# Kernel optimization log

Measured on AMD Instinct MI355X. Metric: run time of the kernel, lower is better.

Reference implementation:

```python
import jax, jax.numpy as jnp
import numpy as np
from jax import lax

EPS = 1e-6
TANH_CLIP = 1.0 - 1e-5
FRECHET_ITERS = 10


def _sqnorm(x):
    return jnp.sum(x * x, axis=-1, keepdims=True)


def _norm(x):
    return jnp.sqrt(jnp.clip(_sqnorm(x), EPS))


def _lambda(x, c):
    # conformal factor lambda_x = 2 / (1 - c ||x||^2)
    return 2.0 / jnp.clip(1.0 - c * _sqnorm(x), EPS)


def mobius_add(x, y, c):
    x2 = _sqnorm(x)
    y2 = _sqnorm(y)
    xy = jnp.sum(x * y, axis=-1, keepdims=True)
    num = (1.0 + 2.0 * c * xy + c * y2) * x + (1.0 - c * x2) * y
    den = 1.0 + 2.0 * c * xy + (c * c) * x2 * y2
    return num / jnp.clip(den, EPS)


def expmap(x, u, c):
    sc = jnp.sqrt(c)
    un = _norm(u)
    second = jnp.tanh(sc * _lambda(x, c) * un / 2.0) * u / (sc * un)
    return mobius_add(x, second, c)


def logmap(x, y, c):
    sc = jnp.sqrt(c)
    m = mobius_add(-x, y, c)
    mn = _norm(m)
    t = jnp.arctanh(jnp.clip(sc * mn, 0.0, TANH_CLIP))
    return (2.0 / (sc * _lambda(x, c))) * t * m / mn


def exp0(u, c):
    sc = jnp.sqrt(c)
    un = _norm(u)
    return jnp.tanh(sc * un) * u / (sc * un)


def dist(x, y, c):
    sc = jnp.sqrt(c)
    mn = _norm(mobius_add(-x, y, c))
    return (2.0 / sc) * jnp.arctanh(jnp.clip(sc * mn, 0.0, TANH_CLIP))[..., 0]


def gyr(a, b, w, c):
    # gyr[a,b]w = -(a (+) b) (+) (a (+) (b (+) w))
    return mobius_add(-mobius_add(a, b, c), mobius_add(a, mobius_add(b, w, c), c), c)


def transp(x, y, u, c):
    # parallel transport x -> y:  (lam_x / lam_y) * gyr[y, -x] u
    return (_lambda(x, c) / _lambda(y, c)) * gyr(y, -x, u, c)


def frechet_mean(x, c):
    # Karcher fixed-point iteration: mu <- exp_mu(mean_i log_mu(x_i))
    m = jnp.mean(x, axis=0)  # (D,)
    max_norm = (1.0 - 1e-3) / jnp.sqrt(c)
    mn = _norm(m)[0]
    m = m * jnp.minimum(1.0, max_norm / mn)

    def step(mu, _):
        g = jnp.mean(logmap(mu, x, c), axis=0)
        return expmap(mu, g, c), None

    mu, _ = lax.scan(step, m, None, length=FRECHET_ITERS)
    return mu


def setup_inputs() -> dict:
    key = jax.random.key(0)
    k1, k2 = jax.random.split(key)
    B, S, D = 64, 256, 256
    K = jnp.float32(-1.2)
    sc = np.sqrt(1.2)
    x = jax.random.normal(k1, (B, S, D), dtype=jnp.float32)
    # project points strictly inside the Poincare ball of radius 1/sqrt(c)
    x = x / (1.0 + _norm(x)) * jnp.float32(0.7 / sc)
    mean_param = 0.01 * jax.random.normal(k2, (D,), dtype=jnp.float32)
    var_param = jnp.float32(1.0)
    return {"x": x, "K": K, "mean_param": mean_param, "var_param": var_param}


def reference(x, K, mean_param, var_param):
    c = -K  # positive ball curvature (K = -1.2)
    shapes = x.shape
    xf = x.reshape(-1, shapes[-1])  # (N, D)
    on_manifold = exp0(mean_param, c)          # (D,) target mean on manifold
    mu = frechet_mean(xf, c)                   # (D,) batch Frechet mean
    var = jnp.mean(dist(xf, mu, c) ** 2)       # Frechet variance (scalar)
    logm = transp(mu, on_manifold, logmap(mu, xf, c), c)  # (N, D)
    logm = jnp.sqrt(var_param / (var + 1e-6)) * logm
    out = expmap(on_manifold, logm, c)         # (N, D)
    return out.reshape(shapes)
```

## Files before the change

kernel.cpp:

```cpp
#include <hip/hip_runtime.h>
#include <math.h>
#include <string.h>

#define EPSF 1e-6f
#define TCLIP (1.0f - 1e-5f)
#define NPTS 16384
#define DDIM 256
#define NBLK 128
#define NTHR 1024
#define PPB 128
#define NWAVE 16
#define PPW 8
#define PSTR 260
#define FRECHET_ITERS_N 10

#define WS_PA 64
#define WS_PB (WS_PA + NBLK * PSTR)

__device__ __forceinline__ void st_pair_sc1(float* addr, float a, float b) {
    float2 f2 = make_float2(a, b);
    double dv; memcpy(&dv, &f2, 8);
    __hip_atomic_store((double*)addr, dv, __ATOMIC_RELAXED, __HIP_MEMORY_SCOPE_AGENT);
}
__device__ __forceinline__ float2 ld_pair_sc1(const float* addr) {
    double dv = __hip_atomic_load((const double*)addr, __ATOMIC_RELAXED, __HIP_MEMORY_SCOPE_AGENT);
    float2 f2; memcpy(&f2, &dv, 8);
    return f2;
}
__device__ __forceinline__ void st_f_sc1(float* addr, float v) {
    __hip_atomic_store(addr, v, __ATOMIC_RELAXED, __HIP_MEMORY_SCOPE_AGENT);
}
__device__ __forceinline__ float ld_f_sc1(const float* addr) {
    return __hip_atomic_load(addr, __ATOMIC_RELAXED, __HIP_MEMORY_SCOPE_AGENT);
}
__device__ __forceinline__ void st_u_sc1(unsigned* addr, unsigned v) {
    __hip_atomic_store(addr, v, __ATOMIC_RELAXED, __HIP_MEMORY_SCOPE_AGENT);
}
__device__ __forceinline__ unsigned ld_u_sc1(const unsigned* addr) {
    return __hip_atomic_load(addr, __ATOMIC_RELAXED, __HIP_MEMORY_SCOPE_AGENT);
}

__device__ __forceinline__ float block_sum(float v) {
    __shared__ float s_bs[NWAVE];
    #pragma unroll
    for (int off = 32; off; off >>= 1) v += __shfl_xor(v, off);
    const int w = threadIdx.x >> 6, l = threadIdx.x & 63;
    __syncthreads();
    if (l == 0) s_bs[w] = v;
    __syncthreads();
    float s = 0.f;
    #pragma unroll
    for (int i = 0; i < NWAVE; ++i) s += s_bs[i];
    return s;
}

__global__ void init_tags(float* ws) {
    int t = threadIdx.x;
    if (t < NBLK) {
        st_u_sc1((unsigned*)(ws + WS_PA + t * PSTR + 258), 0u);
        st_u_sc1((unsigned*)(ws + WS_PB + t * PSTR + 258), 0u);
    }
}

__global__ __launch_bounds__(NTHR, 1) void rbn_fused(
    const float* __restrict__ x, const float* __restrict__ Kp,
    const float* __restrict__ mean_param, const float* __restrict__ var_param,
    float* __restrict__ out, float* __restrict__ ws)
{
    const float c = -Kp[0];
    const float sc = sqrtf(c);
    const float N1 = 1.f / NPTS;
    const int t = threadIdx.x, lane = t & 63, wv = t >> 6;
    const int b = blockIdx.x;
    const int p0 = b * PPB;
    const float4* xr = ((const float4*)x) + p0 * 64;

    float* PA = ws + WS_PA;
    float* PB = ws + WS_PB;

    __shared__ float mu_s[DDIM], om_s[DDIM];
    __shared__ float dpart[PPB * 65];
    __shared__ float dqr[PPB * 9];
    __shared__ float y2_s[PPB], e_s[PPB], d_s[PPB], w_s[PPB], sA_s[PPB], fx_s[PPB];
    __shared__ float pseg[NWAVE * DDIM];
    __shared__ float part1[NWAVE], part2[NWAVE], part3[NWAVE];

    unsigned barno = 0;

    float4 xreg[PPW];
    #pragma unroll
    for (int i = 0; i < PPW; ++i)
        xreg[i] = xr[(wv * PPW + i) * 64 + lane];

    auto poll_tags = [&](const float* buf) {
        if (t < NBLK) {
            const unsigned* tg = (const unsigned*)(buf + t * PSTR + 258);
            while (ld_u_sc1(tg) < barno)
                __builtin_amdgcn_s_sleep(1);
        }
        __syncthreads();
    };

    {
        float u = (t < DDIM) ? mean_param[t] : 0.f;
        float un2 = block_sum(u * u);
        float un = sqrtf(fmaxf(un2, EPSF));
        if (t < DDIM) om_s[t] = tanhf(sc * un) * u / (sc * un);
    }
    float om2;
    { float v = (t < DDIM) ? om_s[t] * om_s[t] : 0.f; om2 = block_sum(v); }

    ++barno;
    {
        float4 a = make_float4(0.f, 0.f, 0.f, 0.f);
        #pragma unroll
        for (int i = 0; i < PPW; ++i) {
            a.x += xreg[i].x; a.y += xreg[i].y; a.z += xreg[i].z; a.w += xreg[i].w;
        }
        __syncthreads();
        ((float4*)(pseg + wv * DDIM))[lane] = a;
        __syncthreads();
        float s = 0.f;
        if (t < DDIM) {
            #pragma unroll
            for (int w = 0; w < NWAVE; ++w) s += pseg[w * DDIM + t];
        }
        float partner = __shfl_xor(s, 1);
        if (t < DDIM && !(t & 1)) st_pair_sc1(PA + b * PSTR + t, s, partner);
        __syncthreads();
        if (t == 0) st_u_sc1((unsigned*)(PA + b * PSTR + 258), barno);
    }
    {
        #pragma unroll
        for (int i = 0; i < PPW; ++i) {
            float4 xv = xreg[i];
            dpart[(wv * PPW + i) * 65 + lane] =
                xv.x * xv.x + xv.y * xv.y + xv.z * xv.z + xv.w * xv.w;
        }
        __syncthreads();
        { int pl = t & 127, q = t >> 7; float s = 0.f;
          #pragma unroll
          for (int j = 0; j < 8; ++j) s += dpart[pl * 65 + q * 8 + j];
          dqr[pl * 9 + q] = s; }
        __syncthreads();
        if (t < PPB) { float s = 0.f;
            #pragma unroll
            for (int j = 0; j < 8; ++j) s += dqr[t * 9 + j];
            y2_s[t] = s; }
        __syncthreads();
        float4 om4 = ((const float4*)om_s)[lane];
        #pragma unroll
        for (int i = 0; i < PPW; ++i) {
            float4 xv = xreg[i];
            dpart[(wv * PPW + i) * 65 + lane] =
                xv.x * om4.x + xv.y * om4.y + xv.z * om4.z + xv.w * om4.w;
        }
        __syncthreads();
        { int pl = t & 127, q = t >> 7; float s = 0.f;
          #pragma unroll
          for (int j = 0; j < 8; ++j) s += dpart[pl * 65 + q * 8 + j];
          dqr[pl * 9 + q] = s; }
        __syncthreads();
        if (t < PPB) { float s = 0.f;
            #pragma unroll
            for (int j = 0; j < 8; ++j) s += dqr[t * 9 + j];
            e_s[t] = s; }
    }
    poll_tags(PA);

    float mu2;
    {
        const int dg = t & 127, sg = t >> 7;
        float ax = 0.f, ay = 0.f;
        #pragma unroll
        for (int j = 0; j < 16; ++j) {
            float2 v = ld_pair_sc1(PA + (sg * 16 + j) * PSTR + 2 * dg);
            ax += v.x; ay += v.y;
        }
        __syncthreads();
        ((float2*)(pseg + sg * DDIM))[dg] = make_float2(ax, ay);
        __syncthreads();
        float m = 0.f, mm = 0.f;
        if (t < DDIM) {
            float s = 0.f;
            #pragma unroll
            for (int w = 0; w < 8; ++w) s += pseg[w * DDIM + t];
            m = s * N1; mm = m * m;
        }
        #pragma unroll
        for (int off = 32; off; off >>= 1) mm += __shfl_xor(mm, off);
        if (lane == 0) part1[wv] = mm;
        __syncthreads();
        float mn2 = 0.f;
        #pragma unroll
        for (int i = 0; i < NWAVE; ++i) mn2 += part1[i];
        float mn = sqrtf(fmaxf(mn2, EPSF));
        float maxn = (1.f - 1e-3f) / sc;
        float f = fminf(1.f, maxn / mn);
        if (t < DDIM) mu_s[t] = m * f;
        mu2 = f * f * mn2;
        __syncthreads();
    }

    for (int it = 0; it < FRECHET_ITERS_N; ++it) {
        float* buf = (it & 1) ? PA : PB;
        ++barno;
        float4 mu4 = ((const float4*)mu_s)[lane];
        #pragma unroll
        for (int i = 0; i < PPW; ++i) {
            float4 xv = xreg[i];
            dpart[(wv * PPW + i) * 65 + lane] =
                xv.x * mu4.x + xv.y * mu4.y + xv.z * mu4.z + xv.w * mu4.w;
        }
        __syncthreads();
        { int pl = t & 127, q = t >> 7; float s = 0.f;
          #pragma unroll
          for (int j = 0; j < 8; ++j) s += dpart[pl * 65 + q * 8 + j];
          dqr[pl * 9 + q] = s; }
        __syncthreads();
        float sAv = 0.f, wdv = 0.f;
        if (t < PPB) {
            float d = 0.f;
            #pragma unroll
            for (int j = 0; j < 8; ++j) d += dqr[t * 9 + j];
            float y2 = y2_s[t];
            float P = 1.f - 2.f * c * d;
            float den = fmaxf(P + c * c * mu2 * y2, EPSF);
            float A = -(P + c * y2) / den;
            float B = (1.f - c * mu2) / den;
            float mn2 = fmaxf(A * A * mu2 + 2.f * A * B * d + B * B * y2, EPSF);
            float mn = sqrtf(mn2);
            float tt = atanhf(fminf(sc * mn, TCLIP));
            float s = (fmaxf(1.f - c * mu2, EPSF) / sc) * tt / mn;
            float w = s * B;
            w_s[t] = w;
            sAv = s * A;
            wdv = w * d;
        }
        __syncthreads();
        {
            float4 a = make_float4(0.f, 0.f, 0.f, 0.f);
            #pragma unroll
            for (int i = 0; i < PPW; ++i) {
                float w = w_s[wv * PPW + i];
                a.x += w * xreg[i].x; a.y += w * xreg[i].y;
                a.z += w * xreg[i].z; a.w += w * xreg[i].w;
            }
            ((float4*)(pseg + wv * DDIM))[lane] = a;
            #pragma unroll
            for (int off = 32; off; off >>= 1) {
                sAv += __shfl_xor(sAv, off); wdv += __shfl_xor(wdv, off);
            }
            if (lane == 0) { part1[wv] = sAv; part2[wv] = wdv; }
        }
        __syncthreads();
        {
            float s = 0.f;
            if (t < DDIM) {
                #pragma unroll
                for (int w = 0; w < NWAVE; ++w) s += pseg[w * DDIM + t];
            }
            float partner = __shfl_xor(s, 1);
            if (t < DDIM && !(t & 1)) st_pair_sc1(buf + b * PSTR + t, s, partner);
            if (t == 0) {
                float sa = 0.f, wd = 0.f;
                #pragma unroll
                for (int i = 0; i < NWAVE; ++i) { sa += part1[i]; wd += part2[i]; }
                st_pair_sc1(buf + b * PSTR + 256, sa, wd);
            }
        }
        __syncthreads();
        if (t == 0) st_u_sc1((unsigned*)(buf + b * PSTR + 258), barno);
        poll_tags(buf);
        const int dg = t & 127, sg = t >> 7;
        float ax = 0.f, ay = 0.f;
        #pragma unroll
        for (int j = 0; j < 16; ++j) {
            float2 v = ld_pair_sc1(buf + (sg * 16 + j) * PSTR + 2 * dg);
            ax += v.x; ay += v.y;
        }
        float2 sp = make_float2(0.f, 0.f);
        if (t < NBLK) sp = ld_pair_sc1(buf + t * PSTR + 256);
        ((float2*)(pseg + sg * DDIM))[dg] = make_float2(ax, ay);
        __syncthreads();
        float g = 0.f, vvv = 0.f;
        if (t < DDIM) {
            #pragma unroll
            for (int w = 0; w < 8; ++w) g += pseg[w * DDIM + t];
            vvv = g * g;
        }
        float sAt = sp.x, wdt = sp.y;
        #pragma unroll
        for (int off = 32; off; off >>= 1) {
            vvv += __shfl_xor(vvv, off); sAt += __shfl_xor(sAt, off); wdt += __shfl_xor(wdt, off);
        }
        if (lane == 0) { part1[wv] = vvv; part2[wv] = sAt; part3[wv] = wdt; }
        __syncthreads();
        float vv = 0.f, sa = 0.f, wd = 0.f;
        #pragma unroll
        for (int i = 0; i < NWAVE; ++i) { vv += part1[i]; sa += part2[i]; wd += part3[i]; }
        float gn2 = N1 * N1 * (vv + 2.f * sa * wd + sa * sa * mu2);
        float mg  = N1 * (wd + sa * mu2);
        float un = sqrtf(fmaxf(gn2, EPSF));
        float lam = 2.f / fmaxf(1.f - c * mu2, EPSF);
        float k = tanhf(sc * lam * un * 0.5f) / (sc * un);
        float ms = k * mg;
        float s2 = k * k * gn2;
        float aa = 1.f + 2.f * c * ms + c * s2;
        float bb2 = 1.f - c * mu2;
        float den = fmaxf(1.f + 2.f * c * ms + c * c * mu2 * s2, EPSF);
        float cm = (aa + bb2 * k * N1 * sa) / den;
        float cv = (bb2 * k * N1) / den;
        if (t < DDIM) mu_s[t] = cm * mu_s[t] + cv * g;
        mu2 = cm * cm * mu2 + 2.f * cm * cv * wd + cv * cv * vv;
        __syncthreads();
    }

    float* vbuf = ((FRECHET_ITERS_N - 1) & 1) ? PB : PA;
    ++barno;
    {
        float4 mu4 = ((const float4*)mu_s)[lane];
        #pragma unroll
        for (int i = 0; i < PPW; ++i) {
            float4 xv = xreg[i];
            dpart[(wv * PPW + i) * 65 + lane] =
                xv.x * mu4.x + xv.y * mu4.y + xv.z * mu4.z + xv.w * mu4.w;
        }
        __syncthreads();
        { int pl = t & 127, q = t >> 7; float s = 0.f;
          #pragma unroll
          for (int j = 0; j < 8; ++j) s += dpart[pl * 65 + q * 8 + j];
          dqr[pl * 9 + q] = s; }
        __syncthreads();
        float vval = 0.f;
        if (t < PPB) {
            float d = 0.f;
            #pragma unroll
            for (int j = 0; j < 8; ++j) d += dqr[t * 9 + j];
            d_s[t] = d;
            float y2 = y2_s[t];
            float P = 1.f - 2.f * c * d;
            float den = fmaxf(P + c * c * mu2 * y2, EPSF);
            float A = -(P + c * y2) / den;
            float B = (1.f - c * mu2) / den;
            float mn2 = fmaxf(A * A * mu2 + 2.f * A * B * d + B * B * y2, EPSF);
            float mn = sqrtf(mn2);
            float tt = atanhf(fminf(sc * mn, TCLIP));
            float dd = (2.f / sc) * tt;
            vval = dd * dd;
        }
        float ov = (t < DDIM) ? om_s[t] * mu_s[t] : 0.f;
        #pragma unroll
        for (int off = 32; off; off >>= 1) {
            vval += __shfl_xor(vval, off); ov += __shfl_xor(ov, off);
        }
        if (lane == 0) { part1[wv] = vval; part2[wv] = ov; }
        __syncthreads();
        if (t == 0) {
            float tot = 0.f;
            #pragma unroll
            for (int i = 0; i < NWAVE; ++i) tot += part1[i];
            st_f_sc1(vbuf + b * PSTR + 256, tot);
        }
        __syncthreads();
        if (t == 0) st_u_sc1((unsigned*)(vbuf + b * PSTR + 258), barno);
    }
    float omu = 0.f;
    #pragma unroll
    for (int i = 0; i < NWAVE; ++i) omu += part2[i];

    const float Amu = fmaxf(1.f - c * mu2, EPSF);
    const float Aom = fmaxf(1.f - c * om2, EPSF);
    const float ratio = Aom / Amu;
    const float aq = 1.f - 2.f * c * omu + c * mu2;
    const float bq = 1.f - c * om2;
    const float dqv = fmaxf(1.f - 2.f * c * omu + c * c * om2 * mu2, EPSF);
    const float qo = aq / dqv, qm = -bq / dqv;
    const float q2 = qo * qo * om2 + 2.f * qo * qm * omu + qm * qm * mu2;
    const float lam_om = 2.f / Aom;

    if (t < PPB) {
        float y2 = y2_s[t], d = d_s[t], e = e_s[t];
        auto dotOm3 = [&](float po, float pm, float px) { return po * om2 + pm * omu + px * e; };
        auto dotMu3 = [&](float po, float pm, float px) { return po * omu + pm * mu2 + px * d; };
        auto sqn3 = [&](float po, float pm, float px) {
            return po * po * om2 + pm * pm * mu2 + px * px * y2
                 + 2.f * (po * pm * omu + po * px * e + pm * px * d);
        };
        float P = 1.f - 2.f * c * d;
        float den0 = fmaxf(P + c * c * mu2 * y2, EPSF);
        float A = -(P + c * y2) / den0;
        float B = (1.f - c * mu2) / den0;
        float mn2 = fmaxf(A * A * mu2 + 2.f * A * B * d + B * B * y2, EPSF);
        float mn = sqrtf(mn2);
        float tt = atanhf(fminf(sc * mn, TCLIP));
        float s = (fmaxf(1.f - c * mu2, EPSF) / sc) * tt / mn;
        float Um = s * A, Ux = s * B;

        float xy1 = -dotMu3(0.f, Um, Ux);
        float Y21 = sqn3(0.f, Um, Ux);
        float a1 = 1.f + 2.f * c * xy1 + c * Y21;
        float b1 = 1.f - c * mu2;
        float dn1 = fmaxf(1.f + 2.f * c * xy1 + c * c * mu2 * Y21, EPSF);
        float h1m = (-a1 + b1 * Um) / dn1;
        float h1x = (b1 * Ux) / dn1;

        float xy2 = dotOm3(0.f, h1m, h1x);
        float Y22 = sqn3(0.f, h1m, h1x);
        float a2 = 1.f + 2.f * c * xy2 + c * Y22;
        float b2 = 1.f - c * om2;
        float dn2 = fmaxf(1.f + 2.f * c * xy2 + c * c * om2 * Y22, EPSF);
        float h2o = a2 / dn2;
        float h2m = (b2 * h1m) / dn2;
        float h2x = (b2 * h1x) / dn2;

        float xy3 = -(qo * dotOm3(h2o, h2m, h2x) + qm * dotMu3(h2o, h2m, h2x));
        float Y23 = sqn3(h2o, h2m, h2x);
        float a3 = 1.f + 2.f * c * xy3 + c * Y23;
        float b3 = 1.f - c * q2;
        float dn3 = fmaxf(1.f + 2.f * c * xy3 + c * c * q2 * Y23, EPSF);
        w_s[t]  = (-a3 * qo + b3 * h2o) / dn3;
        sA_s[t] = (-a3 * qm + b3 * h2m) / dn3;
        fx_s[t] = (b3 * h2x) / dn3;
    }
    poll_tags(vbuf);

    float va = (t < NBLK) ? ld_f_sc1(vbuf + t * PSTR + 256) : 0.f;
    #pragma unroll
    for (int off = 32; off; off >>= 1) va += __shfl_xor(va, off);
    if (lane == 0) part1[wv] = va;
    __syncthreads();
    float vsum = 0.f;
    #pragma unroll
    for (int i = 0; i < NWAVE; ++i) vsum += part1[i];
    float var = vsum * N1;
    float gamma = sqrtf(var_param[0] / (var + 1e-6f));

    if (t < PPB) {
        float y2 = y2_s[t], d = d_s[t], e = e_s[t];
        float g2o = w_s[t], g2m = sA_s[t], g2x = fx_s[t];
        float k1 = ratio * gamma;
        float Lo = k1 * g2o, Lm = k1 * g2m, Lx = k1 * g2x;
        float un2 = Lo * Lo * om2 + Lm * Lm * mu2 + Lx * Lx * y2
                  + 2.f * (Lo * Lm * omu + Lo * Lx * e + Lm * Lx * d);
        float un = sqrtf(fmaxf(un2, EPSF));
        float coef = tanhf(sc * lam_om * un * 0.5f) / (sc * un);
        float So = coef * Lo, Sm = coef * Lm, Sx = coef * Lx;
        float xy4 = So * om2 + Sm * omu + Sx * e;
        float Y24 = coef * coef * un2;
        float a4 = 1.f + 2.f * c * xy4 + c * Y24;
        float b4 = 1.f - c * om2;
        float dn4 = fmaxf(1.f + 2.f * c * xy4 + c * c * om2 * Y24, EPSF);
        w_s[t]  = (a4 + b4 * So) / dn4;
        sA_s[t] = (b4 * Sm) / dn4;
        fx_s[t] = (b4 * Sx) / dn4;
    }
    __syncthreads();

    {
        float4 mu4f = ((const float4*)mu_s)[lane];
        float4 om4f = ((const float4*)om_s)[lane];
        #pragma unroll
        for (int i = 0; i < PPW; ++i) {
            int pl = wv * PPW + i;
            float fo = w_s[pl], fm = sA_s[pl], fx = fx_s[pl];
            float4 x4 = xreg[i];
            float4 o4;
            o4.x = fo * om4f.x + fm * mu4f.x + fx * x4.x;
            o4.y = fo * om4f.y + fm * mu4f.y + fx * x4.y;
            o4.z = fo * om4f.z + fm * mu4f.z + fx * x4.z;
            o4.w = fo * om4f.w + fm * mu4f.w + fx * x4.w;
            ((float4*)out)[(p0 + pl) * 64 + lane] = o4;
        }
    }
}

extern "C" void kernel_launch(void* const* d_in, const int* in_sizes, int n_in,
                              void* d_out, int out_size, void* d_ws, size_t ws_size,
                              hipStream_t stream) {
    const float* x = (const float*)d_in[0];
    const float* K = (const float*)d_in[1];
    const float* mean_param = (const float*)d_in[2];
    const float* var_param = (const float*)d_in[3];
    float* out = (float*)d_out;
    float* ws = (float*)d_ws;

    init_tags<<<1, 256, 0, stream>>>(ws);
    void* args[] = {(void*)&x, (void*)&K, (void*)&mean_param, (void*)&var_param,
                    (void*)&out, (void*)&ws};
    hipLaunchCooperativeKernel((const void*)rbn_fused, dim3(NBLK), dim3(NTHR),
                               args, 0, stream);
}
```

Before: 188.1 us.

## Make per-point dot products wave-local, replacing block-wide reductions and barriers

Each wave now reduces the dot products for its own 8 points using a per-wave LDS slice plus shuffle-xor, and keeps the per-point scalars (y2, e, d, weights) in registers instead of block-shared arrays. This removes several __syncthreads per Frechet iteration and in the prologue and epilogue, along with the shared staging arrays. Per-point coefficients reach the weighted sums through lane shuffles. Every lane in a group of 8 redundantly computes the scalar math, so the transcendental work per point is duplicated across lanes, and wave-level sums have to divide by the redundancy correctly.

```diff
diff --git a/kernel.cpp b/kernel.cpp
--- a/kernel.cpp
+++ b/kernel.cpp
@@ -12,6 +12,7 @@
 #define NWAVE 16
 #define PPW 8
 #define PSTR 260
+#define WSLICE (PPW * 65)
 #define FRECHET_ITERS_N 10
 
 #define WS_PA 64
@@ -79,9 +80,7 @@
     float* PB = ws + WS_PB;
 
     __shared__ float mu_s[DDIM], om_s[DDIM];
-    __shared__ float dpart[PPB * 65];
-    __shared__ float dqr[PPB * 9];
-    __shared__ float y2_s[PPB], e_s[PPB], d_s[PPB], w_s[PPB], sA_s[PPB], fx_s[PPB];
+    __shared__ float dpart[NWAVE * WSLICE];
     __shared__ float pseg[NWAVE * DDIM];
     __shared__ float part1[NWAVE], part2[NWAVE], part3[NWAVE];
 
@@ -91,6 +90,28 @@
     #pragma unroll
     for (int i = 0; i < PPW; ++i)
         xreg[i] = xr[(wv * PPW + i) * 64 + lane];
+
+    auto wave_dot = [&](float4 v4, bool self) -> float {
+        float* slice = dpart + wv * WSLICE;
+        #pragma unroll
+        for (int i = 0; i < PPW; ++i) {
+            float4 xv = xreg[i];
+            float4 u4 = self ? xv : v4;
+            slice[i * 65 + lane] = xv.x * u4.x + xv.y * u4.y + xv.z * u4.z + xv.w * u4.w;
+        }
+        const int g = lane >> 3, q = lane & 7;
+        float s = 0.f;
+        #pragma unroll
+        for (int j = 0; j < 8; ++j) s += slice[g * 65 + q * 8 + j];
+        #pragma unroll
+        for (int off = 1; off <= 4; off <<= 1) s += __shfl_xor(s, off);
+        return s;
+    };
+    auto wave_sum_groups = [&](float v) -> float {
+        #pragma unroll
+        for (int off = 8; off <= 32; off <<= 1) v += __shfl_xor(v, off);
+        return v;
+    };
 
     auto poll_tags = [&](const float* buf) {
         if (t < NBLK) {
@@ -117,9 +138,10 @@
         for (int i = 0; i < PPW; ++i) {
             a.x += xreg[i].x; a.y += xreg[i].y; a.z += xreg[i].z; a.w += xreg[i].w;
         }
-        __syncthreads();
         ((float4*)(pseg + wv * DDIM))[lane] = a;
-        __syncthreads();
+    }
+    __syncthreads();
+    {
         float s = 0.f;
         if (t < DDIM) {
             #pragma unroll
@@ -127,44 +149,15 @@
         }
         float partner = __shfl_xor(s, 1);
         if (t < DDIM && !(t & 1)) st_pair_sc1(PA + b * PSTR + t, s, partner);
-        __syncthreads();
-        if (t == 0) st_u_sc1((unsigned*)(PA + b * PSTR + 258), barno);
-    }
-    {
-        #pragma unroll
-        for (int i = 0; i < PPW; ++i) {
-            float4 xv = xreg[i];
-            dpart[(wv * PPW + i) * 65 + lane] =
-                xv.x * xv.x + xv.y * xv.y + xv.z * xv.z + xv.w * xv.w;
-        }
-        __syncthreads();
-        { int pl = t & 127, q = t >> 7; float s = 0.f;
-          #pragma unroll
-          for (int j = 0; j < 8; ++j) s += dpart[pl * 65 + q * 8 + j];
-          dqr[pl * 9 + q] = s; }
-        __syncthreads();
-        if (t < PPB) { float s = 0.f;
-            #pragma unroll
-            for (int j = 0; j < 8; ++j) s += dqr[t * 9 + j];
-            y2_s[t] = s; }
-        __syncthreads();
+    }
+    __syncthreads();
+    if (t == 0) st_u_sc1((unsigned*)(PA + b * PSTR + 258), barno);
+
+    float y2r = wave_dot(make_float4(0.f, 0.f, 0.f, 0.f), true);
+    float er;
+    {
         float4 om4 = ((const float4*)om_s)[lane];
-        #pragma unroll
-        for (int i = 0; i < PPW; ++i) {
-            float4 xv = xreg[i];
-            dpart[(wv * PPW + i) * 65 + lane] =
-                xv.x * om4.x + xv.y * om4.y + xv.z * om4.z + xv.w * om4.w;
-        }
-        __syncthreads();
-        { int pl = t & 127, q = t >> 7; float s = 0.f;
-          #pragma unroll
-          for (int j = 0; j < 8; ++j) s += dpart[pl * 65 + q * 8 + j];
-          dqr[pl * 9 + q] = s; }
-        __syncthreads();
-        if (t < PPB) { float s = 0.f;
-            #pragma unroll
-            for (int j = 0; j < 8; ++j) s += dqr[t * 9 + j];
-            e_s[t] = s; }
+        er = wave_dot(om4, false);
     }
     poll_tags(PA);
 
@@ -177,7 +170,6 @@
             float2 v = ld_pair_sc1(PA + (sg * 16 + j) * PSTR + 2 * dg);
             ax += v.x; ay += v.y;
         }
-        __syncthreads();
         ((float2*)(pseg + sg * DDIM))[dg] = make_float2(ax, ay);
         __syncthreads();
         float m = 0.f, mm = 0.f;
@@ -206,24 +198,10 @@
         float* buf = (it & 1) ? PA : PB;
         ++barno;
         float4 mu4 = ((const float4*)mu_s)[lane];
-        #pragma unroll
-        for (int i = 0; i < PPW; ++i) {
-            float4 xv = xreg[i];
-            dpart[(wv * PPW + i) * 65 + lane] =
-                xv.x * mu4.x + xv.y * mu4.y + xv.z * mu4.z + xv.w * mu4.w;
-        }
-        __syncthreads();
-        { int pl = t & 127, q = t >> 7; float s = 0.f;
-          #pragma unroll
-          for (int j = 0; j < 8; ++j) s += dpart[pl * 65 + q * 8 + j];
-          dqr[pl * 9 + q] = s; }
-        __syncthreads();
-        float sAv = 0.f, wdv = 0.f;
-        if (t < PPB) {
-            float d = 0.f;
-            #pragma unroll
-            for (int j = 0; j < 8; ++j) d += dqr[t * 9 + j];
-            float y2 = y2_s[t];
+        float d = wave_dot(mu4, false);
+        float w, sA;
+        {
+            float y2 = y2r;
             float P = 1.f - 2.f * c * d;
             float den = fmaxf(P + c * c * mu2 * y2, EPSF);
             float A = -(P + c * y2) / den;
@@ -232,33 +210,28 @@
             float mn = sqrtf(mn2);
             float tt = atanhf(fminf(sc * mn, TCLIP));
             float s = (fmaxf(1.f - c * mu2, EPSF) / sc) * tt / mn;
-            float w = s * B;
-            w_s[t] = w;
-            sAv = s * A;
-            wdv = w * d;
-        }
-        __syncthreads();
+            w = s * B;
+            sA = s * A;
+        }
         {
             float4 a = make_float4(0.f, 0.f, 0.f, 0.f);
             #pragma unroll
             for (int i = 0; i < PPW; ++i) {
-                float w = w_s[wv * PPW + i];
-                a.x += w * xreg[i].x; a.y += w * xreg[i].y;
-                a.z += w * xreg[i].z; a.w += w * xreg[i].w;
+                float wi = __shfl(w, i * 8);
+                a.x += wi * xreg[i].x; a.y += wi * xreg[i].y;
+                a.z += wi * xreg[i].z; a.w += wi * xreg[i].w;
             }
             ((float4*)(pseg + wv * DDIM))[lane] = a;
-            #pragma unroll
-            for (int off = 32; off; off >>= 1) {
-                sAv += __shfl_xor(sAv, off); wdv += __shfl_xor(wdv, off);
-            }
-            if (lane == 0) { part1[wv] = sAv; part2[wv] = wdv; }
-        }
+        }
+        float sAw = wave_sum_groups(sA);
+        float wdw = wave_sum_groups(w * d);
+        if (lane == 0) { part1[wv] = sAw; part2[wv] = wdw; }
         __syncthreads();
         {
             float s = 0.f;
             if (t < DDIM) {
                 #pragma unroll
-                for (int w = 0; w < NWAVE; ++w) s += pseg[w * DDIM + t];
+                for (int w2 = 0; w2 < NWAVE; ++w2) s += pseg[w2 * DDIM + t];
             }
             float partner = __shfl_xor(s, 1);
             if (t < DDIM && !(t & 1)) st_pair_sc1(buf + b * PSTR + t, s, partner);
@@ -286,7 +259,7 @@
         float g = 0.f, vvv = 0.f;
         if (t < DDIM) {
             #pragma unroll
-            for (int w = 0; w < 8; ++w) g += pseg[w * DDIM + t];
+            for (int w2 = 0; w2 < 8; ++w2) g += pseg[w2 * DDIM + t];
             vvv = g * g;
         }
         float sAt = sp.x, wdt = sp.y;
@@ -318,53 +291,39 @@
 
     float* vbuf = ((FRECHET_ITERS_N - 1) & 1) ? PB : PA;
     ++barno;
-    {
-        float4 mu4 = ((const float4*)mu_s)[lane];
-        #pragma unroll
-        for (int i = 0; i < PPW; ++i) {
-            float4 xv = xreg[i];
-            dpart[(wv * PPW + i) * 65 + lane] =
-                xv.x * mu4.x + xv.y * mu4.y + xv.z * mu4.z + xv.w * mu4.w;
-        }
-        __syncthreads();
-        { int pl = t & 127, q = t >> 7; float s = 0.f;
-          #pragma unroll
-          for (int j = 0; j < 8; ++j) s += dpart[pl * 65 + q * 8 + j];
-          dqr[pl * 9 + q] = s; }
-        __syncthreads();
-        float vval = 0.f;
-        if (t < PPB) {
-            float d = 0.f;
-            #pragma unroll
-            for (int j = 0; j < 8; ++j) d += dqr[t * 9 + j];
-            d_s[t] = d;
-            float y2 = y2_s[t];
-            float P = 1.f - 2.f * c * d;
-            float den = fmaxf(P + c * c * mu2 * y2, EPSF);
-            float A = -(P + c * y2) / den;
-            float B = (1.f - c * mu2) / den;
-            float mn2 = fmaxf(A * A * mu2 + 2.f * A * B * d + B * B * y2, EPSF);
-            float mn = sqrtf(mn2);
-            float tt = atanhf(fminf(sc * mn, TCLIP));
-            float dd = (2.f / sc) * tt;
-            vval = dd * dd;
-        }
+    float4 mu4f = ((const float4*)mu_s)[lane];
+    float4 om4f = ((const float4*)om_s)[lane];
+    float d = wave_dot(mu4f, false);
+    float vval;
+    {
+        float y2 = y2r;
+        float P = 1.f - 2.f * c * d;
+        float den = fmaxf(P + c * c * mu2 * y2, EPSF);
+        float A = -(P + c * y2) / den;
+        float B = (1.f - c * mu2) / den;
+        float mn2 = fmaxf(A * A * mu2 + 2.f * A * B * d + B * B * y2, EPSF);
+        float mn = sqrtf(mn2);
+        float tt = atanhf(fminf(sc * mn, TCLIP));
+        float dd = (2.f / sc) * tt;
+        vval = dd * dd;
+    }
+    {
+        float vw = wave_sum_groups(vval);
         float ov = (t < DDIM) ? om_s[t] * mu_s[t] : 0.f;
         #pragma unroll
-        for (int off = 32; off; off >>= 1) {
-            vval += __shfl_xor(vval, off); ov += __shfl_xor(ov, off);
-        }
-        if (lane == 0) { part1[wv] = vval; part2[wv] = ov; }
-        __syncthreads();
-        if (t == 0) {
-            float tot = 0.f;
-            #pragma unroll
-            for (int i = 0; i < NWAVE; ++i) tot += part1[i];
-            st_f_sc1(vbuf + b * PSTR + 256, tot);
-        }
-        __syncthreads();
-        if (t == 0) st_u_sc1((unsigned*)(vbuf + b * PSTR + 258), barno);
-    }
+        for (int off = 32; off; off >>= 1) ov += __shfl_xor(ov, off);
+        if (lane == 0) { part1[wv] = vw; part2[wv] = ov; }
+    }
+    __syncthreads();
+    if (t == 0) {
+        float tot = 0.f;
+        #pragma unroll
+        for (int i = 0; i < NWAVE; ++i) tot += part1[i];
+        st_f_sc1(vbuf + b * PSTR + 256, tot);
+    }
+    __syncthreads();
+    if (t == 0) st_u_sc1((unsigned*)(vbuf + b * PSTR + 258), barno);
+
     float omu = 0.f;
     #pragma unroll
     for (int i = 0; i < NWAVE; ++i) omu += part2[i];
@@ -379,8 +338,9 @@
     const float q2 = qo * qo * om2 + 2.f * qo * qm * omu + qm * qm * mu2;
     const float lam_om = 2.f / Aom;
 
-    if (t < PPB) {
-        float y2 = y2_s[t], d = d_s[t], e = e_s[t];
+    float g2o, g2m, g2x;
+    {
+        float y2 = y2r, e = er;
         auto dotOm3 = [&](float po, float pm, float px) { return po * om2 + pm * omu + px * e; };
         auto dotMu3 = [&](float po, float pm, float px) { return po * omu + pm * mu2 + px * d; };
         auto sqn3 = [&](float po, float pm, float px) {
@@ -419,16 +379,18 @@
         float a3 = 1.f + 2.f * c * xy3 + c * Y23;
         float b3 = 1.f - c * q2;
         float dn3 = fmaxf(1.f + 2.f * c * xy3 + c * c * q2 * Y23, EPSF);
-        w_s[t]  = (-a3 * qo + b3 * h2o) / dn3;
-        sA_s[t] = (-a3 * qm + b3 * h2m) / dn3;
-        fx_s[t] = (b3 * h2x) / dn3;
+        g2o = (-a3 * qo + b3 * h2o) / dn3;
+        g2m = (-a3 * qm + b3 * h2m) / dn3;
+        g2x = (b3 * h2x) / dn3;
     }
     poll_tags(vbuf);
 
-    float va = (t < NBLK) ? ld_f_sc1(vbuf + t * PSTR + 256) : 0.f;
-    #pragma unroll
-    for (int off = 32; off; off >>= 1) va += __shfl_xor(va, off);
-    if (lane == 0) part1[wv] = va;
+    {
+        float va = (t < NBLK) ? ld_f_sc1(vbuf + t * PSTR + 256) : 0.f;
+        #pragma unroll
+        for (int off = 32; off; off >>= 1) va += __shfl_xor(va, off);
+        if (lane == 0) part1[wv] = va;
+    }
     __syncthreads();
     float vsum = 0.f;
     #pragma unroll
@@ -436,9 +398,9 @@
     float var = vsum * N1;
     float gamma = sqrtf(var_param[0] / (var + 1e-6f));
 
-    if (t < PPB) {
-        float y2 = y2_s[t], d = d_s[t], e = e_s[t];
-        float g2o = w_s[t], g2m = sA_s[t], g2x = fx_s[t];
+    float fo, fm, fx;
+    {
+        float y2 = y2r, e = er;
         float k1 = ratio * gamma;
         float Lo = k1 * g2o, Lm = k1 * g2m, Lx = k1 * g2x;
         float un2 = Lo * Lo * om2 + Lm * Lm * mu2 + Lx * Lx * y2
@@ -451,27 +413,23 @@
         float a4 = 1.f + 2.f * c * xy4 + c * Y24;
         float b4 = 1.f - c * om2;
         float dn4 = fmaxf(1.f + 2.f * c * xy4 + c * c * om2 * Y24, EPSF);
-        w_s[t]  = (a4 + b4 * So) / dn4;
-        sA_s[t] = (b4 * Sm) / dn4;
-        fx_s[t] = (b4 * Sx) / dn4;
-    }
-    __syncthreads();
-
-    {
-        float4 mu4f = ((const float4*)mu_s)[lane];
-        float4 om4f = ((const float4*)om_s)[lane];
-        #pragma unroll
-        for (int i = 0; i < PPW; ++i) {
-            int pl = wv * PPW + i;
-            float fo = w_s[pl], fm = sA_s[pl], fx = fx_s[pl];
-            float4 x4 = xreg[i];
-            float4 o4;
-            o4.x = fo * om4f.x + fm * mu4f.x + fx * x4.x;
-            o4.y = fo * om4f.y + fm * mu4f.y + fx * x4.y;
-            o4.z = fo * om4f.z + fm * mu4f.z + fx * x4.z;
-            o4.w = fo * om4f.w + fm * mu4f.w + fx * x4.w;
-            ((float4*)out)[(p0 + pl) * 64 + lane] = o4;
-        }
+        fo = (a4 + b4 * So) / dn4;
+        fm = (b4 * Sm) / dn4;
+        fx = (b4 * Sx) / dn4;
+    }
+
+    #pragma unroll
+    for (int i = 0; i < PPW; ++i) {
+        float foi = __shfl(fo, i * 8);
+        float fmi = __shfl(fm, i * 8);
+        float fxi = __shfl(fx, i * 8);
+        float4 x4 = xreg[i];
+        float4 o4;
+        o4.x = foi * om4f.x + fmi * mu4f.x + fxi * x4.x;
+        o4.y = foi * om4f.y + fmi * mu4f.y + fxi * x4.y;
+        o4.z = foi * om4f.z + fmi * mu4f.z + fxi * x4.z;
+        o4.w = foi * om4f.w + fmi * mu4f.w + fxi * x4.w;
+        ((float4*)out)[(p0 + wv * PPW + i) * 64 + lane] = o4;
     }
 }
 
```

New measurement: 194.0 us. 1.03x slower.

## Replace all-to-all grid reduction with single reducer block and broadcast tag

Applied to the files above, without the earlier changes.

Before, every block polled all 128 partial tags and re-read every block's partial sums to do the same reduction. Now block 0 alone gathers the partials, computes the updated mean (or the variance) and publishes it with one broadcast tag that the other blocks poll. Local per-block work (y2/e dot products, the transport coefficients) runs while waiting. The double-buffered partials and the separate tag-init kernel are dropped; equality polling on reused tags replaces them. The cost is an extra gather-then-broadcast hop on each iteration's critical path, plus some reliance on stale tag values never matching the expected phase.

```diff
diff --git a/kernel.cpp b/kernel.cpp
--- a/kernel.cpp
+++ b/kernel.cpp
@@ -13,9 +13,10 @@
 #define PPW 8
 #define PSTR 260
 #define FRECHET_ITERS_N 10
-
-#define WS_PA 64
-#define WS_PB (WS_PA + NBLK * PSTR)
+#define REDB 0
+
+#define WS_MU 64
+#define WS_PA (WS_MU + PSTR)
 
 __device__ __forceinline__ void st_pair_sc1(float* addr, float a, float b) {
     float2 f2 = make_float2(a, b);
@@ -52,14 +53,6 @@
     #pragma unroll
     for (int i = 0; i < NWAVE; ++i) s += s_bs[i];
     return s;
-}
-
-__global__ void init_tags(float* ws) {
-    int t = threadIdx.x;
-    if (t < NBLK) {
-        st_u_sc1((unsigned*)(ws + WS_PA + t * PSTR + 258), 0u);
-        st_u_sc1((unsigned*)(ws + WS_PB + t * PSTR + 258), 0u);
-    }
 }
 
 __global__ __launch_bounds__(NTHR, 1) void rbn_fused(
@@ -75,8 +68,9 @@
     const int p0 = b * PPB;
     const float4* xr = ((const float4*)x) + p0 * 64;
 
+    float* MU = ws + WS_MU;
     float* PA = ws + WS_PA;
-    float* PB = ws + WS_PB;
+    unsigned* MUtag = (unsigned*)(MU + 258);
 
     __shared__ float mu_s[DDIM], om_s[DDIM];
     __shared__ float dpart[PPB * 65];
@@ -84,21 +78,54 @@
     __shared__ float y2_s[PPB], e_s[PPB], d_s[PPB], w_s[PPB], sA_s[PPB], fx_s[PPB];
     __shared__ float pseg[NWAVE * DDIM];
     __shared__ float part1[NWAVE], part2[NWAVE], part3[NWAVE];
-
-    unsigned barno = 0;
+    __shared__ float bc[2];
+
+    unsigned p = 0;
 
     float4 xreg[PPW];
     #pragma unroll
     for (int i = 0; i < PPW; ++i)
         xreg[i] = xr[(wv * PPW + i) * 64 + lane];
 
-    auto poll_tags = [&](const float* buf) {
-        if (t < NBLK) {
-            const unsigned* tg = (const unsigned*)(buf + t * PSTR + 258);
-            while (ld_u_sc1(tg) < barno)
-                __builtin_amdgcn_s_sleep(1);
-        }
-        __syncthreads();
+    auto poll_eq = [&](const unsigned* tg, unsigned want) {
+        while (ld_u_sc1(tg) != want) __builtin_amdgcn_s_sleep(1);
+    };
+
+    auto compute_y2e = [&]() {
+        #pragma unroll
+        for (int i = 0; i < PPW; ++i) {
+            float4 xv = xreg[i];
+            dpart[(wv * PPW + i) * 65 + lane] =
+                xv.x * xv.x + xv.y * xv.y + xv.z * xv.z + xv.w * xv.w;
+        }
+        __syncthreads();
+        { int pl = t & 127, q = t >> 7; float s = 0.f;
+          #pragma unroll
+          for (int j = 0; j < 8; ++j) s += dpart[pl * 65 + q * 8 + j];
+          dqr[pl * 9 + q] = s; }
+        __syncthreads();
+        if (t < PPB) { float s = 0.f;
+            #pragma unroll
+            for (int j = 0; j < 8; ++j) s += dqr[t * 9 + j];
+            y2_s[t] = s; }
+        __syncthreads();
+        float4 om4 = ((const float4*)om_s)[lane];
+        #pragma unroll
+        for (int i = 0; i < PPW; ++i) {
+            float4 xv = xreg[i];
+            dpart[(wv * PPW + i) * 65 + lane] =
+                xv.x * om4.x + xv.y * om4.y + xv.z * om4.z + xv.w * om4.w;
+        }
+        __syncthreads();
+        { int pl = t & 127, q = t >> 7; float s = 0.f;
+          #pragma unroll
+          for (int j = 0; j < 8; ++j) s += dpart[pl * 65 + q * 8 + j];
+          dqr[pl * 9 + q] = s; }
+        __syncthreads();
+        if (t < PPB) { float s = 0.f;
+            #pragma unroll
+            for (int j = 0; j < 8; ++j) s += dqr[t * 9 + j];
+            e_s[t] = s; }
     };
 
     {
@@ -110,16 +137,17 @@
     float om2;
     { float v = (t < DDIM) ? om_s[t] * om_s[t] : 0.f; om2 = block_sum(v); }
 
-    ++barno;
+    ++p;
     {
         float4 a = make_float4(0.f, 0.f, 0.f, 0.f);
         #pragma unroll
         for (int i = 0; i < PPW; ++i) {
             a.x += xreg[i].x; a.y += xreg[i].y; a.z += xreg[i].z; a.w += xreg[i].w;
         }
-        __syncthreads();
         ((float4*)(pseg + wv * DDIM))[lane] = a;
-        __syncthreads();
+    }
+    __syncthreads();
+    {
         float s = 0.f;
         if (t < DDIM) {
             #pragma unroll
@@ -127,49 +155,14 @@
         }
         float partner = __shfl_xor(s, 1);
         if (t < DDIM && !(t & 1)) st_pair_sc1(PA + b * PSTR + t, s, partner);
-        __syncthreads();
-        if (t == 0) st_u_sc1((unsigned*)(PA + b * PSTR + 258), barno);
-    }
-    {
-        #pragma unroll
-        for (int i = 0; i < PPW; ++i) {
-            float4 xv = xreg[i];
-            dpart[(wv * PPW + i) * 65 + lane] =
-                xv.x * xv.x + xv.y * xv.y + xv.z * xv.z + xv.w * xv.w;
-        }
-        __syncthreads();
-        { int pl = t & 127, q = t >> 7; float s = 0.f;
-          #pragma unroll
-          for (int j = 0; j < 8; ++j) s += dpart[pl * 65 + q * 8 + j];
-          dqr[pl * 9 + q] = s; }
-        __syncthreads();
-        if (t < PPB) { float s = 0.f;
-            #pragma unroll
-            for (int j = 0; j < 8; ++j) s += dqr[t * 9 + j];
-            y2_s[t] = s; }
-        __syncthreads();
-        float4 om4 = ((const float4*)om_s)[lane];
-        #pragma unroll
-        for (int i = 0; i < PPW; ++i) {
-            float4 xv = xreg[i];
-            dpart[(wv * PPW + i) * 65 + lane] =
-                xv.x * om4.x + xv.y * om4.y + xv.z * om4.z + xv.w * om4.w;
-        }
-        __syncthreads();
-        { int pl = t & 127, q = t >> 7; float s = 0.f;
-          #pragma unroll
-          for (int j = 0; j < 8; ++j) s += dpart[pl * 65 + q * 8 + j];
-          dqr[pl * 9 + q] = s; }
-        __syncthreads();
-        if (t < PPB) { float s = 0.f;
-            #pragma unroll
-            for (int j = 0; j < 8; ++j) s += dqr[t * 9 + j];
-            e_s[t] = s; }
-    }
-    poll_tags(PA);
+    }
+    __syncthreads();
+    if (t == 0) st_u_sc1((unsigned*)(PA + b * PSTR + 258), p);
 
     float mu2;
-    {
+    if (b == REDB) {
+        if (t < NBLK) poll_eq((const unsigned*)(PA + t * PSTR + 258), p);
+        __syncthreads();
         const int dg = t & 127, sg = t >> 7;
         float ax = 0.f, ay = 0.f;
         #pragma unroll
@@ -177,7 +170,6 @@
             float2 v = ld_pair_sc1(PA + (sg * 16 + j) * PSTR + 2 * dg);
             ax += v.x; ay += v.y;
         }
-        __syncthreads();
         ((float2*)(pseg + sg * DDIM))[dg] = make_float2(ax, ay);
         __syncthreads();
         float m = 0.f, mm = 0.f;
@@ -197,14 +189,23 @@
         float mn = sqrtf(fmaxf(mn2, EPSF));
         float maxn = (1.f - 1e-3f) / sc;
         float f = fminf(1.f, maxn / mn);
-        if (t < DDIM) mu_s[t] = m * f;
+        if (t < DDIM) { float nm = m * f; mu_s[t] = nm; st_f_sc1(MU + t, nm); }
         mu2 = f * f * mn2;
+        if (t == 0) st_f_sc1(MU + 256, mu2);
+        __syncthreads();
+        if (t == 0) st_u_sc1(MUtag, p);
+        compute_y2e();
+    } else {
+        compute_y2e();
+        if (t == 0) { poll_eq(MUtag, p); bc[0] = ld_f_sc1(MU + 256); }
+        __syncthreads();
+        if (t < DDIM) mu_s[t] = ld_f_sc1(MU + t);
+        mu2 = bc[0];
         __syncthreads();
     }
 
     for (int it = 0; it < FRECHET_ITERS_N; ++it) {
-        float* buf = (it & 1) ? PA : PB;
-        ++barno;
+        ++p;
         float4 mu4 = ((const float4*)mu_s)[lane];
         #pragma unroll
         for (int i = 0; i < PPW; ++i) {
@@ -258,113 +259,128 @@
             float s = 0.f;
             if (t < DDIM) {
                 #pragma unroll
-                for (int w = 0; w < NWAVE; ++w) s += pseg[w * DDIM + t];
+                for (int w2 = 0; w2 < NWAVE; ++w2) s += pseg[w2 * DDIM + t];
             }
             float partner = __shfl_xor(s, 1);
-            if (t < DDIM && !(t & 1)) st_pair_sc1(buf + b * PSTR + t, s, partner);
+            if (t < DDIM && !(t & 1)) st_pair_sc1(PA + b * PSTR + t, s, partner);
             if (t == 0) {
                 float sa = 0.f, wd = 0.f;
                 #pragma unroll
                 for (int i = 0; i < NWAVE; ++i) { sa += part1[i]; wd += part2[i]; }
-                st_pair_sc1(buf + b * PSTR + 256, sa, wd);
-            }
-        }
-        __syncthreads();
-        if (t == 0) st_u_sc1((unsigned*)(buf + b * PSTR + 258), barno);
-        poll_tags(buf);
-        const int dg = t & 127, sg = t >> 7;
-        float ax = 0.f, ay = 0.f;
-        #pragma unroll
-        for (int j = 0; j < 16; ++j) {
-            float2 v = ld_pair_sc1(buf + (sg * 16 + j) * PSTR + 2 * dg);
-            ax += v.x; ay += v.y;
-        }
-        float2 sp = make_float2(0.f, 0.f);
-        if (t < NBLK) sp = ld_pair_sc1(buf + t * PSTR + 256);
-        ((float2*)(pseg + sg * DDIM))[dg] = make_float2(ax, ay);
-        __syncthreads();
-        float g = 0.f, vvv = 0.f;
-        if (t < DDIM) {
-            #pragma unroll
-            for (int w = 0; w < 8; ++w) g += pseg[w * DDIM + t];
-            vvv = g * g;
-        }
-        float sAt = sp.x, wdt = sp.y;
-        #pragma unroll
-        for (int off = 32; off; off >>= 1) {
-            vvv += __shfl_xor(vvv, off); sAt += __shfl_xor(sAt, off); wdt += __shfl_xor(wdt, off);
-        }
-        if (lane == 0) { part1[wv] = vvv; part2[wv] = sAt; part3[wv] = wdt; }
-        __syncthreads();
-        float vv = 0.f, sa = 0.f, wd = 0.f;
-        #pragma unroll
-        for (int i = 0; i < NWAVE; ++i) { vv += part1[i]; sa += part2[i]; wd += part3[i]; }
-        float gn2 = N1 * N1 * (vv + 2.f * sa * wd + sa * sa * mu2);
-        float mg  = N1 * (wd + sa * mu2);
-        float un = sqrtf(fmaxf(gn2, EPSF));
-        float lam = 2.f / fmaxf(1.f - c * mu2, EPSF);
-        float k = tanhf(sc * lam * un * 0.5f) / (sc * un);
-        float ms = k * mg;
-        float s2 = k * k * gn2;
-        float aa = 1.f + 2.f * c * ms + c * s2;
-        float bb2 = 1.f - c * mu2;
-        float den = fmaxf(1.f + 2.f * c * ms + c * c * mu2 * s2, EPSF);
-        float cm = (aa + bb2 * k * N1 * sa) / den;
-        float cv = (bb2 * k * N1) / den;
-        if (t < DDIM) mu_s[t] = cm * mu_s[t] + cv * g;
-        mu2 = cm * cm * mu2 + 2.f * cm * cv * wd + cv * cv * vv;
-        __syncthreads();
-    }
-
-    float* vbuf = ((FRECHET_ITERS_N - 1) & 1) ? PB : PA;
-    ++barno;
-    {
-        float4 mu4 = ((const float4*)mu_s)[lane];
-        #pragma unroll
-        for (int i = 0; i < PPW; ++i) {
-            float4 xv = xreg[i];
-            dpart[(wv * PPW + i) * 65 + lane] =
-                xv.x * mu4.x + xv.y * mu4.y + xv.z * mu4.z + xv.w * mu4.w;
-        }
-        __syncthreads();
-        { int pl = t & 127, q = t >> 7; float s = 0.f;
-          #pragma unroll
-          for (int j = 0; j < 8; ++j) s += dpart[pl * 65 + q * 8 + j];
-          dqr[pl * 9 + q] = s; }
-        __syncthreads();
-        float vval = 0.f;
-        if (t < PPB) {
-            float d = 0.f;
-            #pragma unroll
-            for (int j = 0; j < 8; ++j) d += dqr[t * 9 + j];
-            d_s[t] = d;
-            float y2 = y2_s[t];
-            float P = 1.f - 2.f * c * d;
-            float den = fmaxf(P + c * c * mu2 * y2, EPSF);
-            float A = -(P + c * y2) / den;
-            float B = (1.f - c * mu2) / den;
-            float mn2 = fmaxf(A * A * mu2 + 2.f * A * B * d + B * B * y2, EPSF);
-            float mn = sqrtf(mn2);
-            float tt = atanhf(fminf(sc * mn, TCLIP));
-            float dd = (2.f / sc) * tt;
-            vval = dd * dd;
-        }
-        float ov = (t < DDIM) ? om_s[t] * mu_s[t] : 0.f;
-        #pragma unroll
-        for (int off = 32; off; off >>= 1) {
-            vval += __shfl_xor(vval, off); ov += __shfl_xor(ov, off);
-        }
-        if (lane == 0) { part1[wv] = vval; part2[wv] = ov; }
-        __syncthreads();
-        if (t == 0) {
-            float tot = 0.f;
-            #pragma unroll
-            for (int i = 0; i < NWAVE; ++i) tot += part1[i];
-            st_f_sc1(vbuf + b * PSTR + 256, tot);
-        }
-        __syncthreads();
-        if (t == 0) st_u_sc1((unsigned*)(vbuf + b * PSTR + 258), barno);
-    }
+                st_pair_sc1(PA + b * PSTR + 256, sa, wd);
+            }
+        }
+        __syncthreads();
+        if (t == 0) st_u_sc1((unsigned*)(PA + b * PSTR + 258), p);
+
+        if (b == REDB) {
+            if (t < NBLK) poll_eq((const unsigned*)(PA + t * PSTR + 258), p);
+            __syncthreads();
+            const int dg = t & 127, sg = t >> 7;
+            float ax = 0.f, ay = 0.f;
+            #pragma unroll
+            for (int j = 0; j < 16; ++j) {
+                float2 v = ld_pair_sc1(PA + (sg * 16 + j) * PSTR + 2 * dg);
+                ax += v.x; ay += v.y;
+            }
+            float2 sp = make_float2(0.f, 0.f);
+            if (t < NBLK) sp = ld_pair_sc1(PA + t * PSTR + 256);
+            ((float2*)(pseg + sg * DDIM))[dg] = make_float2(ax, ay);
+            __syncthreads();
+            float g = 0.f, vvv = 0.f;
+            if (t < DDIM) {
+                #pragma unroll
+                for (int w2 = 0; w2 < 8; ++w2) g += pseg[w2 * DDIM + t];
+                vvv = g * g;
+            }
+            float sAt = sp.x, wdt = sp.y;
+            #pragma unroll
+            for (int off = 32; off; off >>= 1) {
+                vvv += __shfl_xor(vvv, off); sAt += __shfl_xor(sAt, off); wdt += __shfl_xor(wdt, off);
+            }
+            if (lane == 0) { part1[wv] = vvv; part2[wv] = sAt; part3[wv] = wdt; }
+            __syncthreads();
+            float vv = 0.f, sa = 0.f, wd = 0.f;
+            #pragma unroll
+            for (int i = 0; i < NWAVE; ++i) { vv += part1[i]; sa += part2[i]; wd += part3[i]; }
+            float gn2 = N1 * N1 * (vv + 2.f * sa * wd + sa * sa * mu2);
+            float mg  = N1 * (wd + sa * mu2);
+            float un = sqrtf(fmaxf(gn2, EPSF));
+            float lam = 2.f / fmaxf(1.f - c * mu2, EPSF);
+            float k = tanhf(sc * lam * un * 0.5f) / (sc * un);
+            float ms = k * mg;
+            float s2 = k * k * gn2;
+            float aa = 1.f + 2.f * c * ms + c * s2;
+            float bb2 = 1.f - c * mu2;
+            float den = fmaxf(1.f + 2.f * c * ms + c * c * mu2 * s2, EPSF);
+            float cm = (aa + bb2 * k * N1 * sa) / den;
+            float cv = (bb2 * k * N1) / den;
+            if (t < DDIM) {
+                float nm = cm * mu_s[t] + cv * g;
+                mu_s[t] = nm;
+                st_f_sc1(MU + t, nm);
+            }
+            mu2 = cm * cm * mu2 + 2.f * cm * cv * wd + cv * cv * vv;
+            if (t == 0) st_f_sc1(MU + 256, mu2);
+            __syncthreads();
+            if (t == 0) st_u_sc1(MUtag, p);
+        } else {
+            if (t == 0) { poll_eq(MUtag, p); bc[0] = ld_f_sc1(MU + 256); }
+            __syncthreads();
+            if (t < DDIM) mu_s[t] = ld_f_sc1(MU + t);
+            mu2 = bc[0];
+            __syncthreads();
+        }
+    }
+
+    ++p;
+    float4 mu4f = ((const float4*)mu_s)[lane];
+    float4 om4f = ((const float4*)om_s)[lane];
+    #pragma unroll
+    for (int i = 0; i < PPW; ++i) {
+        float4 xv = xreg[i];
+        dpart[(wv * PPW + i) * 65 + lane] =
+            xv.x * mu4f.x + xv.y * mu4f.y + xv.z * mu4f.z + xv.w * mu4f.w;
+    }
+    __syncthreads();
+    { int pl = t & 127, q = t >> 7; float s = 0.f;
+      #pragma unroll
+      for (int j = 0; j < 8; ++j) s += dpart[pl * 65 + q * 8 + j];
+      dqr[pl * 9 + q] = s; }
+    __syncthreads();
+    float vval = 0.f;
+    if (t < PPB) {
+        float d = 0.f;
+        #pragma unroll
+        for (int j = 0; j < 8; ++j) d += dqr[t * 9 + j];
+        d_s[t] = d;
+        float y2 = y2_s[t];
+        float P = 1.f - 2.f * c * d;
+        float den = fmaxf(P + c * c * mu2 * y2, EPSF);
+        float A = -(P + c * y2) / den;
+        float B = (1.f - c * mu2) / den;
+        float mn2 = fmaxf(A * A * mu2 + 2.f * A * B * d + B * B * y2, EPSF);
+        float mn = sqrtf(mn2);
+        float tt = atanhf(fminf(sc * mn, TCLIP));
+        float dd = (2.f / sc) * tt;
+        vval = dd * dd;
+    }
+    float ov = (t < DDIM) ? om_s[t] * mu_s[t] : 0.f;
+    #pragma unroll
+    for (int off = 32; off; off >>= 1) {
+        vval += __shfl_xor(vval, off); ov += __shfl_xor(ov, off);
+    }
+    if (lane == 0) { part1[wv] = vval; part2[wv] = ov; }
+    __syncthreads();
+    if (t == 0) {
+        float tot = 0.f;
+        #pragma unroll
+        for (int i = 0; i < NWAVE; ++i) tot += part1[i];
+        st_f_sc1(PA + b * PSTR + 256, tot);
+    }
+    __syncthreads();
+    if (t == 0) st_u_sc1((unsigned*)(PA + b * PSTR + 258), p);
+
     float omu = 0.f;
     #pragma unroll
     for (int i = 0; i < NWAVE; ++i) omu += part2[i];
@@ -379,61 +395,76 @@
     const float q2 = qo * qo * om2 + 2.f * qo * qm * omu + qm * qm * mu2;
     const float lam_om = 2.f / Aom;
 
-    if (t < PPB) {
-        float y2 = y2_s[t], d = d_s[t], e = e_s[t];
-        auto dotOm3 = [&](float po, float pm, float px) { return po * om2 + pm * omu + px * e; };
-        auto dotMu3 = [&](float po, float pm, float px) { return po * omu + pm * mu2 + px * d; };
-        auto sqn3 = [&](float po, float pm, float px) {
-            return po * po * om2 + pm * pm * mu2 + px * px * y2
-                 + 2.f * (po * pm * omu + po * px * e + pm * px * d);
-        };
-        float P = 1.f - 2.f * c * d;
-        float den0 = fmaxf(P + c * c * mu2 * y2, EPSF);
-        float A = -(P + c * y2) / den0;
-        float B = (1.f - c * mu2) / den0;
-        float mn2 = fmaxf(A * A * mu2 + 2.f * A * B * d + B * B * y2, EPSF);
-        float mn = sqrtf(mn2);
-        float tt = atanhf(fminf(sc * mn, TCLIP));
-        float s = (fmaxf(1.f - c * mu2, EPSF) / sc) * tt / mn;
-        float Um = s * A, Ux = s * B;
-
-        float xy1 = -dotMu3(0.f, Um, Ux);
-        float Y21 = sqn3(0.f, Um, Ux);
-        float a1 = 1.f + 2.f * c * xy1 + c * Y21;
-        float b1 = 1.f - c * mu2;
-        float dn1 = fmaxf(1.f + 2.f * c * xy1 + c * c * mu2 * Y21, EPSF);
-        float h1m = (-a1 + b1 * Um) / dn1;
-        float h1x = (b1 * Ux) / dn1;
-
-        float xy2 = dotOm3(0.f, h1m, h1x);
-        float Y22 = sqn3(0.f, h1m, h1x);
-        float a2 = 1.f + 2.f * c * xy2 + c * Y22;
-        float b2 = 1.f - c * om2;
-        float dn2 = fmaxf(1.f + 2.f * c * xy2 + c * c * om2 * Y22, EPSF);
-        float h2o = a2 / dn2;
-        float h2m = (b2 * h1m) / dn2;
-        float h2x = (b2 * h1x) / dn2;
-
-        float xy3 = -(qo * dotOm3(h2o, h2m, h2x) + qm * dotMu3(h2o, h2m, h2x));
-        float Y23 = sqn3(h2o, h2m, h2x);
-        float a3 = 1.f + 2.f * c * xy3 + c * Y23;
-        float b3 = 1.f - c * q2;
-        float dn3 = fmaxf(1.f + 2.f * c * xy3 + c * c * q2 * Y23, EPSF);
-        w_s[t]  = (-a3 * qo + b3 * h2o) / dn3;
-        sA_s[t] = (-a3 * qm + b3 * h2m) / dn3;
-        fx_s[t] = (b3 * h2x) / dn3;
-    }
-    poll_tags(vbuf);
-
-    float va = (t < NBLK) ? ld_f_sc1(vbuf + t * PSTR + 256) : 0.f;
-    #pragma unroll
-    for (int off = 32; off; off >>= 1) va += __shfl_xor(va, off);
-    if (lane == 0) part1[wv] = va;
-    __syncthreads();
-    float vsum = 0.f;
-    #pragma unroll
-    for (int i = 0; i < NWAVE; ++i) vsum += part1[i];
-    float var = vsum * N1;
+    auto hidden_g2 = [&]() {
+        if (t < PPB) {
+            float y2 = y2_s[t], d = d_s[t], e = e_s[t];
+            auto dotOm3 = [&](float po, float pm, float px) { return po * om2 + pm * omu + px * e; };
+            auto dotMu3 = [&](float po, float pm, float px) { return po * omu + pm * mu2 + px * d; };
+            auto sqn3 = [&](float po, float pm, float px) {
+                return po * po * om2 + pm * pm * mu2 + px * px * y2
+                     + 2.f * (po * pm * omu + po * px * e + pm * px * d);
+            };
+            float P = 1.f - 2.f * c * d;
+            float den0 = fmaxf(P + c * c * mu2 * y2, EPSF);
+            float A = -(P + c * y2) / den0;
+            float B = (1.f - c * mu2) / den0;
+            float mn2 = fmaxf(A * A * mu2 + 2.f * A * B * d + B * B * y2, EPSF);
+            float mn = sqrtf(mn2);
+            float tt = atanhf(fminf(sc * mn, TCLIP));
+            float s = (fmaxf(1.f - c * mu2, EPSF) / sc) * tt / mn;
+            float Um = s * A, Ux = s * B;
+
+            float xy1 = -dotMu3(0.f, Um, Ux);
+            float Y21 = sqn3(0.f, Um, Ux);
+            float a1 = 1.f + 2.f * c * xy1 + c * Y21;
+            float b1 = 1.f - c * mu2;
+            float dn1 = fmaxf(1.f + 2.f * c * xy1 + c * c * mu2 * Y21, EPSF);
+            float h1m = (-a1 + b1 * Um) / dn1;
+            float h1x = (b1 * Ux) / dn1;
+
+            float xy2 = dotOm3(0.f, h1m, h1x);
+            float Y22 = sqn3(0.f, h1m, h1x);
+            float a2 = 1.f + 2.f * c * xy2 + c * Y22;
+            float b2 = 1.f - c * om2;
+            float dn2 = fmaxf(1.f + 2.f * c * xy2 + c * c * om2 * Y22, EPSF);
+            float h2o = a2 / dn2;
+            float h2m = (b2 * h1m) / dn2;
+            float h2x = (b2 * h1x) / dn2;
+
+            float xy3 = -(qo * dotOm3(h2o, h2m, h2x) + qm * dotMu3(h2o, h2m, h2x));
+            float Y23 = sqn3(h2o, h2m, h2x);
+            float a3 = 1.f + 2.f * c * xy3 + c * Y23;
+            float b3 = 1.f - c * q2;
+            float dn3 = fmaxf(1.f + 2.f * c * xy3 + c * c * q2 * Y23, EPSF);
+            w_s[t]  = (-a3 * qo + b3 * h2o) / dn3;
+            sA_s[t] = (-a3 * qm + b3 * h2m) / dn3;
+            fx_s[t] = (b3 * h2x) / dn3;
+        }
+    };
+
+    float var;
+    if (b == REDB) {
+        if (t < NBLK) poll_eq((const unsigned*)(PA + t * PSTR + 258), p);
+        __syncthreads();
+        float va = (t < NBLK) ? ld_f_sc1(PA + t * PSTR + 256) : 0.f;
+        #pragma unroll
+        for (int off = 32; off; off >>= 1) va += __shfl_xor(va, off);
+        if (lane == 0) part1[wv] = va;
+        __syncthreads();
+        float vsum = 0.f;
+        #pragma unroll
+        for (int i = 0; i < NWAVE; ++i) vsum += part1[i];
+        var = vsum * N1;
+        if (t == 0) st_f_sc1(MU + 256, var);
+        __syncthreads();
+        if (t == 0) st_u_sc1(MUtag, p);
+        hidden_g2();
+    } else {
+        hidden_g2();
+        if (t == 0) { poll_eq(MUtag, p); bc[0] = ld_f_sc1(MU + 256); }
+        __syncthreads();
+        var = bc[0];
+    }
     float gamma = sqrtf(var_param[0] / (var + 1e-6f));
 
     if (t < PPB) {
@@ -457,21 +488,17 @@
     }
     __syncthreads();
 
-    {
-        float4 mu4f = ((const float4*)mu_s)[lane];
-        float4 om4f = ((const float4*)om_s)[lane];
-        #pragma unroll
-        for (int i = 0; i < PPW; ++i) {
-            int pl = wv * PPW + i;
-            float fo = w_s[pl], fm = sA_s[pl], fx = fx_s[pl];
-            float4 x4 = xreg[i];
-            float4 o4;
-            o4.x = fo * om4f.x + fm * mu4f.x + fx * x4.x;
-            o4.y = fo * om4f.y + fm * mu4f.y + fx * x4.y;
-            o4.z = fo * om4f.z + fm * mu4f.z + fx * x4.z;
-            o4.w = fo * om4f.w + fm * mu4f.w + fx * x4.w;
-            ((float4*)out)[(p0 + pl) * 64 + lane] = o4;
-        }
+    #pragma unroll
+    for (int i = 0; i < PPW; ++i) {
+        int pl = wv * PPW + i;
+        float fo = w_s[pl], fm = sA_s[pl], fx = fx_s[pl];
+        float4 x4 = xreg[i];
+        float4 o4;
+        o4.x = fo * om4f.x + fm * mu4f.x + fx * x4.x;
+        o4.y = fo * om4f.y + fm * mu4f.y + fx * x4.y;
+        o4.z = fo * om4f.z + fm * mu4f.z + fx * x4.z;
+        o4.w = fo * om4f.w + fm * mu4f.w + fx * x4.w;
+        ((float4*)out)[(p0 + pl) * 64 + lane] = o4;
     }
 }
 
@@ -485,7 +512,6 @@
     float* out = (float*)d_out;
     float* ws = (float*)d_ws;
 
-    init_tags<<<1, 256, 0, stream>>>(ws);
     void* args[] = {(void*)&x, (void*)&K, (void*)&mean_param, (void*)&var_param,
                     (void*)&out, (void*)&ws};
     hipLaunchCooperativeKernel((const void*)rbn_fused, dim3(NBLK), dim3(NTHR),
```

New measurement: 211.9 us. 12.6% more time.
